# Kernel optimization log

Hardware: AMD Instinct MI355X
Metric: run time of the kernel (lower is better)

## Reference

```python
import jax, jax.numpy as jnp
import numpy as np

C_IN = 1024
C_MID = 512  # in_channels // shrink_factor


def conv1x1(x, w, b):
    # x: [B, Cin, H, W], w: [Cout, Cin], b: [Cout]
    return jnp.einsum('bchw,oc->bohw', x, w) + b[None, :, None, None]


def setup_inputs() -> dict:
    key = jax.random.key(0)
    ks = jax.random.split(key, 9)
    B, H, W = 8, 48, 48
    x = jax.random.normal(ks[0], (B, C_IN, H, W), dtype=jnp.float32)
    s = 0.02
    w1 = jax.random.normal(ks[1], (C_MID, C_IN), dtype=jnp.float32) * s
    b1 = jnp.zeros((C_MID,), dtype=jnp.float32)
    w2 = jax.random.normal(ks[2], (C_MID, C_IN), dtype=jnp.float32) * s
    b2 = jnp.zeros((C_MID,), dtype=jnp.float32)
    w3 = jax.random.normal(ks[3], (C_MID, C_IN), dtype=jnp.float32) * s
    b3 = jnp.zeros((C_MID,), dtype=jnp.float32)
    w4 = jax.random.normal(ks[4], (C_IN, C_MID), dtype=jnp.float32) * s
    b4 = jnp.zeros((C_IN,), dtype=jnp.float32)
    return {'x': x, 'w1': w1, 'b1': b1, 'w2': w2, 'b2': b2,
            'w3': w3, 'b3': b3, 'w4': w4, 'b4': b4}


def reference(x, w1, b1, w2, b2, w3, b3, w4, b4):
    B, C, H, W = x.shape
    # 1x1 conv projections (theta, phi, g), each [B, C_MID, H, W]
    x_theta = conv1x1(x, w1, b1)
    x_phi = conv1x1(x, w2, b2)
    x_g = conv1x1(x, w3, b3)
    # NOTE: the original uses raw .view() (no transpose); torch and jnp are both
    # row-major, so jnp.reshape reproduces the exact same memory reinterpretation.
    x_g = x_g.reshape(B, -1, C_MID)      # [B, N, C_MID]
    x_theta = x_theta.reshape(B, -1, C_MID)  # [B, N, C_MID]
    x_phi = x_phi.reshape(B, C_MID, -1)  # [B, C_MID, N]
    # full dense N x N affinity (N = H*W)
    att = jnp.einsum('bnc,bcm->bnm', x_theta, x_phi)
    att = jax.nn.softmax(att, axis=-1)
    y = jnp.einsum('bnm,bmc->bnc', att, x_g)  # [B, N, C_MID]
    y = y.reshape(B, C_MID, H, W)
    x_last = conv1x1(y, w4, b4)  # [B, C_IN, H, W]
    return x + x_last
```

## Files before the change

### kernel.cpp

```cpp
#include <hip/hip_runtime.h>

typedef unsigned short u16;
typedef __bf16 bf16x8_t __attribute__((ext_vector_type(8)));
typedef float f32x4_t __attribute__((ext_vector_type(4)));

__device__ __forceinline__ u16 f2bf(float f) {
  unsigned u = __builtin_bit_cast(unsigned, f);
  u += 0x7FFFu + ((u >> 16) & 1u);
  return (u16)(u >> 16);
}
__device__ __forceinline__ float bf2f(u16 h) {
  unsigned u = ((unsigned)h) << 16;
  return __builtin_bit_cast(float, u);
}

typedef __attribute__((address_space(1))) const unsigned gas_u32;
typedef __attribute__((address_space(3))) unsigned las_u32;
__device__ __forceinline__ void gload16(const void* g, void* l) {
  __builtin_amdgcn_global_load_lds((gas_u32*)g, (las_u32*)l, 16, 0, 0);
}

#define SBAR()                                  \
  do {                                          \
    __builtin_amdgcn_sched_barrier(0);          \
    asm volatile("" ::: "memory");              \
    __builtin_amdgcn_s_barrier();               \
    asm volatile("" ::: "memory");              \
    __builtin_amdgcn_sched_barrier(0);          \
  } while (0)
#define VM10() asm volatile("s_waitcnt vmcnt(10)" ::: "memory")
#define VM12() asm volatile("s_waitcnt vmcnt(12)" ::: "memory")

__global__ __launch_bounds__(256) void cast4_kernel(
    const float* __restrict__ a0, const float* __restrict__ a1,
    const float* __restrict__ a2, const float* __restrict__ a3,
    u16* __restrict__ out) {
  const int z = blockIdx.z;
  const float* a = (z == 0) ? a0 : (z == 1) ? a1 : (z == 2) ? a2 : a3;
  const int i = blockIdx.x * 256 + threadIdx.x;
  out[(size_t)z * 524288 + i] = f2bf(a[i]);
}

__global__ __launch_bounds__(256) void bcat_kernel(
    const float* __restrict__ b1, const float* __restrict__ b3,
    float* __restrict__ o) {
  const int i = blockIdx.x * 256 + threadIdx.x;
  o[i] = (i < 512) ? b1[i] : b3[i - 512];
}

__global__ __launch_bounds__(256) void cast_transpose_kernel(
    const float* __restrict__ in, u16* __restrict__ out, int R, int C,
    long sIn, long sOut) {
  __shared__ u16 t[32][33];
  const int b = blockIdx.z;
  in += (long)b * sIn;
  out += (long)b * sOut;
  const int c0 = blockIdx.x * 32, r0 = blockIdx.y * 32;
  const int tx = threadIdx.x, ty = threadIdx.y;
#pragma unroll
  for (int i = 0; i < 32; i += 8)
    t[ty + i][tx] = f2bf(in[(long)(r0 + ty + i) * C + c0 + tx]);
  __syncthreads();
#pragma unroll
  for (int i = 0; i < 32; i += 8)
    out[(long)(c0 + ty + i) * R + r0 + tx] = t[tx][ty + i];
}

__global__ __launch_bounds__(256) void transpose64(
    const u16* __restrict__ in, u16* __restrict__ out, int R, int C, long sIn,
    long sOut) {
  __shared__ u16 t[64][66];
  const int b = blockIdx.z;
  in += (long)b * sIn;
  out += (long)b * sOut;
  const int c0 = blockIdx.x * 64, r0 = blockIdx.y * 64;
  const int tx = threadIdx.x & 31, ty = threadIdx.x >> 5;
#pragma unroll
  for (int i = 0; i < 64; i += 8) {
    unsigned v = *(const unsigned*)&in[(long)(r0 + ty + i) * C + c0 + 2 * tx];
    t[ty + i][2 * tx] = (u16)v;
    t[ty + i][2 * tx + 1] = (u16)(v >> 16);
  }
  __syncthreads();
#pragma unroll
  for (int i = 0; i < 64; i += 8) {
    unsigned lo = t[2 * tx][ty + i], hi = t[2 * tx + 1][ty + i];
    *(unsigned*)&out[(long)(c0 + ty + i) * R + r0 + 2 * tx] = lo | (hi << 16);
  }
}

#define STG_A(bufv, h, kt)                                          \
  do {                                                              \
    const char* g_ = Ag + (size_t)(kt) * 128 + (size_t)(h)*AH;      \
    char* d_ = sAd + (bufv)*32768 + (h)*16384;                      \
    gload16(g_, d_);                                                \
    gload16(g_ + AC, d_ + 8192);                                    \
  } while (0)
#define STG_B(bufv, h, kt)                                          \
  do {                                                              \
    const char* g_ = Bg + (size_t)(kt) * 128 + (size_t)(h)*BH;      \
    char* d_ = sBd + (bufv)*32768 + (h)*16384;                      \
    gload16(g_, d_);                                                \
    gload16(g_ + BC, d_ + 8192);                                    \
  } while (0)
#define LOAD_A(bufv, mh)                                                     \
  _Pragma("unroll") for (int m = 0; m < 4; m++) {                            \
    const int lr_ = (mh)*128 + wr * 64 + m * 16 + l15;                       \
    af[m][0] = *(const bf16x8_t*)(lds + (bufv)*32768 + lr_ * 128 + koff0);   \
    af[m][1] =                                                               \
        *(const bf16x8_t*)(lds + (bufv)*32768 + lr_ * 128 + (koff0 ^ 64));   \
  }
#define LOAD_B(bufv, nh)                                                     \
  _Pragma("unroll") for (int n = 0; n < 2; n++) {                            \
    const int lr_ = (nh)*128 + wc * 32 + n * 16 + l15;                       \
    bfr[(nh)*2 + n][0] =                                                     \
        *(const bf16x8_t*)(lds + 65536 + (bufv)*32768 + lr_ * 128 + koff0);  \
    bfr[(nh)*2 + n][1] = *(const bf16x8_t*)(lds + 65536 + (bufv)*32768 +     \
                                            lr_ * 128 + (koff0 ^ 64));       \
  }
#define MMA(mh, nh)                                                          \
  __builtin_amdgcn_s_setprio(1);                                            \
  _Pragma("unroll") for (int m = 0; m < 4; m++)                              \
      _Pragma("unroll") for (int n = 0; n < 2; n++)                          \
          _Pragma("unroll") for (int kk = 0; kk < 2; kk++)                   \
              acc[(mh)*4 + m][(nh)*2 + n] =                                  \
      __builtin_amdgcn_mfma_f32_16x16x32_bf16(                               \
          af[m][kk], bfr[(nh)*2 + n][kk], acc[(mh)*4 + m][(nh)*2 + n], 0, 0, \
          0);                                                                \
  __builtin_amdgcn_s_setprio(0);

template <int MODE>
__global__ __launch_bounds__(512, 2) void gemm8(
    const u16* __restrict__ A, const u16* __restrict__ B,
    void* __restrict__ C0, void* __restrict__ C1, void* __restrict__ C2,
    const u16* __restrict__ W2, const float* __restrict__ bias,
    const float* __restrict__ bias2, const float* __restrict__ resid,
    float* __restrict__ stats) {
  constexpr int LDA_ = (MODE == 0) ? 1024 : (MODE == 3) ? 2304 : 512;
  constexpr int LDB_ = (MODE == 0) ? 1024 : (MODE == 3) ? 2304 : 512;
  constexpr int KK = (MODE == 0) ? 1024 : (MODE == 3) ? 2304 : 512;
  constexpr int NT = KK >> 6;
  constexpr size_t AH = 64ull * LDA_ * 2, AC = 128ull * LDA_ * 2;
  constexpr size_t BH = 32ull * LDB_ * 2, BC = 128ull * LDB_ * 2;

  __shared__ alignas(16) char lds[131072];
  const int tid = threadIdx.x;
  const int w = tid >> 6, l = tid & 63;
  const int wr = w >> 2, wc = w & 3;
  const int l15 = l & 15, lhi = l >> 4;
  const int koff0 = (lhi * 16) ^ ((l & 7) << 4);

  unsigned bx, by, bz;
  bool roleB = false;
  if constexpr (MODE == 0) {
    unsigned bid = blockIdx.x;
    unsigned swz = (bid & 7u) * 54u + (bid >> 3);
    roleB = (swz >= 288u);
    unsigned s = roleB ? swz - 288u : swz;
    if (roleB) { bx = s % 2u; by = (s / 2u) % 9u; bz = s / 18u; }
    else       { bx = s % 9u; by = (s / 9u) % 4u; bz = s / 36u; }
  } else {
    const unsigned gx = gridDim.x, gy = gridDim.y;
    const unsigned nb = gx * gy * gridDim.z;
    unsigned bid = blockIdx.x + gx * (blockIdx.y + gy * blockIdx.z);
    bid = (bid & 7u) * (nb >> 3) + (bid >> 3);
    bx = bid % gx;
    unsigned t1 = bid / gx;
    by = t1 % gy;
    bz = t1 / gy;
  }
  const int rowbase = by * 256, colbase = bx * 256;

  const u16* Abase;
  const u16* Bbase;
  if constexpr (MODE == 0) {
    Abase = roleB ? (B + (size_t)bz * 2359296) : A;
    Bbase = roleB ? W2 : (B + (size_t)bz * 2359296);
  } else if constexpr (MODE == 1) {
    Abase = A + (size_t)bz * 1179648;
    Bbase = B + (size_t)bz * 1179648;
  } else if constexpr (MODE == 3) {
    Abase = A + (size_t)bz * 5308416;
    Bbase = B + (size_t)bz * 1179648;
  } else {
    Abase = A;
    Bbase = B + (size_t)bz * 1179648;
  }

  const int sub = tid >> 3;
  const int kb = ((tid & 7) * 16) ^ ((sub & 7) << 4);
  const char* Ag = (const char*)(Abase + (size_t)(rowbase + sub) * LDA_) + kb;
  const char* Bg =
      (const char*)(Bbase + (size_t)(colbase + (sub >> 5) * 64 + (sub & 31)) *
                                LDB_) +
      kb;
  char* sAd = lds + w * 1024;
  char* sBd = lds + 65536 + w * 1024;

  f32x4_t acc[8][4] = {};
  bf16x8_t af[4][2], bfr[4][2];

  STG_A(0, 0, 0); STG_B(0, 0, 0);
  STG_B(0, 1, 0); STG_A(0, 1, 0);
  STG_A(1, 0, 1); STG_B(1, 0, 1);
  STG_B(1, 1, 1); STG_A(1, 1, 1);
  VM12();
  SBAR();

  for (int t = 0; t < NT; ++t) {
    const int c = t & 1;
    const int tn2 = (t + 2 < NT) ? t + 2 : NT - 1;
    LOAD_A(c, 0);
    LOAD_B(c, 0);
    SBAR();
    MMA(0, 0);
    VM10();
    SBAR();
    LOAD_B(c, 1);
    STG_A(c, 0, tn2);
    STG_B(c, 0, tn2);
    SBAR();
    MMA(0, 1);
    VM12();
    SBAR();
    LOAD_A(c, 1);
    STG_B(c, 1, tn2);
    SBAR();
    MMA(1, 0);
    SBAR();
    STG_A(c, 1, tn2);
    VM12();
    SBAR();
    MMA(1, 1);
    SBAR();
  }

  if constexpr (MODE == 0) {
    if (!roleB) {
      const int rb = rowbase + wr * 128;
      const int which = rb >> 9;
      u16* Cp = (u16*)(which ? C1 : C0) + (size_t)bz * 1179648;
      const int rowout0 = rb - which * 512;
#pragma unroll
      for (int mf = 0; mf < 8; mf++)
#pragma unroll
        for (int r = 0; r < 4; r++) {
          const int ro = mf * 16 + lhi * 4 + r;
          const float bv = bias[rb + ro];
          const size_t rowo = (size_t)(rowout0 + ro) * 2304;
#pragma unroll
          for (int nf = 0; nf < 4; nf++) {
            const int col = colbase + wc * 64 + nf * 16 + l15;
            Cp[rowo + col] = f2bf(acc[mf][nf][r] + bv);
          }
        }
    } else {
      u16* Cp = (u16*)C2 + (size_t)bz * 1179648;
#pragma unroll
      for (int mf = 0; mf < 8; mf++)
#pragma unroll
        for (int r = 0; r < 4; r++) {
          const size_t rowo =
              (size_t)(rowbase + wr * 128 + mf * 16 + lhi * 4 + r) * 512;
#pragma unroll
          for (int nf = 0; nf < 4; nf++) {
            const int col = colbase + wc * 64 + nf * 16 + l15;
            Cp[rowo + col] = f2bf(acc[mf][nf][r] + bias2[col]);
          }
        }
    }
  } else if constexpr (MODE == 1) {
    u16* Cp = (u16*)C0 + (size_t)bz * 5308416;
#pragma unroll
    for (int mf = 0; mf < 8; mf++)
#pragma unroll
      for (int r = 0; r < 4; r++) {
        const int row = rowbase + wr * 128 + mf * 16 + lhi * 4 + r;
        float sm = 0.f;
#pragma unroll
        for (int nf = 0; nf < 4; nf++) {
          const int col = colbase + wc * 64 + nf * 16 + l15;
          const u16 hb = f2bf(__expf(acc[mf][nf][r]));
          Cp[(size_t)row * 2304 + col] = hb;
          sm += bf2f(hb);
        }
#pragma unroll
        for (int mk = 1; mk < 16; mk <<= 1) sm += __shfl_xor(sm, mk);
        if (l15 == 0)
          stats[((size_t)bz * 36 + bx * 4 + wc) * 2304 + row] = sm;
      }
  } else if constexpr (MODE == 3) {
    u16* Cp = (u16*)C0 + (size_t)bz * 1179648;
#pragma unroll
    for (int mf = 0; mf < 8; mf++)
#pragma unroll
      for (int r = 0; r < 4; r++) {
        const int row = rowbase + wr * 128 + mf * 16 + lhi * 4 + r;
        const float invs = stats[(size_t)bz * 2304 + row];
#pragma unroll
        for (int nf = 0; nf < 4; nf++) {
          const int col = colbase + wc * 64 + nf * 16 + l15;
          Cp[(size_t)row * 512 + col] = f2bf(acc[mf][nf][r] * invs);
        }
      }
  } else {
    float* Cp = (float*)C0 + (size_t)bz * 2359296;
    const float* rp = resid + (size_t)bz * 2359296;
#pragma unroll
    for (int mf = 0; mf < 8; mf++)
#pragma unroll
      for (int r = 0; r < 4; r++) {
        const int row = rowbase + wr * 128 + mf * 16 + lhi * 4 + r;
        const float bv = bias[row];
#pragma unroll
        for (int nf = 0; nf < 4; nf++) {
          const int col = colbase + wc * 64 + nf * 16 + l15;
          Cp[(size_t)row * 2304 + col] =
              acc[mf][nf][r] + bv + rp[(size_t)row * 2304 + col];
        }
      }
  }
}

__global__ __launch_bounds__(256) void reduce_sums(
    const float* __restrict__ stats, float* __restrict__ rowinv) {
  const int i = blockIdx.x * 256 + threadIdx.x;
  const int bz = i / 2304, n = i % 2304;
  const float* s = stats + (size_t)bz * 36 * 2304 + n;
  float S = 0.f;
  for (int j = 0; j < 36; j++) S += s[(size_t)j * 2304];
  rowinv[i] = 1.0f / S;
}

extern "C" void kernel_launch(void* const* d_in, const int* in_sizes, int n_in,
                              void* d_out, int out_size, void* d_ws,
                              size_t ws_size, hipStream_t stream) {
  const float* x = (const float*)d_in[0];
  const float* w1 = (const float*)d_in[1];
  const float* b1 = (const float*)d_in[2];
  const float* w2 = (const float*)d_in[3];
  const float* b2 = (const float*)d_in[4];
  const float* w3 = (const float*)d_in[5];
  const float* b3 = (const float*)d_in[6];
  const float* w4 = (const float*)d_in[7];
  const float* b4 = (const float*)d_in[8];
  float* out = (float*)d_out;
  char* ws = (char*)d_ws;

  if (ws_size < 268435456ull) return;
  u16* p_xT = (u16*)(ws);
  u16* p_gn = (u16*)(ws + 37748736);
  float* p_bcat = (float*)(ws + 56623104);
  u16* p_att = (u16*)(ws);
  float* p_stats = (float*)(ws + 84934656);
  float* p_rinv = (float*)(ws + 87588864);
  u16* p_wb = (u16*)(ws + 169869312);
  u16* p_theta = (u16*)(ws + 174063616);
  u16* p_phiT = (u16*)(ws + 192937984);
  u16* p_gT = (u16*)(ws + 211812352);
  u16* p_y = (u16*)(ws + 230686720);
  u16* p_yrT = (u16*)(ws + 249561088);

  cast4_kernel<<<dim3(2048, 1, 4), 256, 0, stream>>>(w1, w3, w2, w4, p_wb);
  bcat_kernel<<<dim3(4), 256, 0, stream>>>(b1, b3, p_bcat);
  cast_transpose_kernel<<<dim3(72, 32, 8), dim3(32, 8), 0, stream>>>(
      x, p_xT, 1024, 2304, 2359296L, 2359296L);
  gemm8<0><<<dim3(432), 512, 0, stream>>>(
      p_wb, p_xT, p_theta, p_gn, p_phiT, p_wb + 1048576, p_bcat, b2, nullptr,
      nullptr);
  transpose64<<<dim3(8, 36, 8), 256, 0, stream>>>(p_gn, p_gT, 2304, 512,
                                                  1179648L, 1179648L);
  gemm8<1><<<dim3(9, 9, 8), 512, 0, stream>>>(
      p_theta, p_phiT, p_att, nullptr, nullptr, nullptr, nullptr, nullptr,
      nullptr, p_stats);
  reduce_sums<<<dim3(72), 256, 0, stream>>>(p_stats, p_rinv);
  gemm8<3><<<dim3(2, 9, 8), 512, 0, stream>>>(
      p_att, p_gT, p_y, nullptr, nullptr, nullptr, nullptr, nullptr, nullptr,
      p_rinv);
  transpose64<<<dim3(36, 8, 8), 256, 0, stream>>>(p_y, p_yrT, 512, 2304,
                                                  1179648L, 1179648L);
  gemm8<2><<<dim3(9, 4, 8), 512, 0, stream>>>(
      p_wb + 1572864, p_yrT, out, nullptr, nullptr, nullptr, b4, nullptr, x,
      nullptr);
}
```

Baseline: 309.9 us.

## Stage GEMM epilogues through LDS for coalesced vector global stores

All GEMM epilogue modes now write accumulator tiles into LDS first, then read them back as 16-byte vectors, so each global store (and the fp32 residual load) is fully coalesced instead of scattered 2- or 4-byte writes. The exp-softmax mode also computes row partial sums over the whole 256-column block tile, cutting the stats partials from 36 to 9 per row, and the reduction kernel is updated to match. This adds LDS round trips, extra barriers and a full vmcnt drain before the epilogue.

```diff
diff --git a/kernel.cpp b/kernel.cpp
--- a/kernel.cpp
+++ b/kernel.cpp
@@ -2,6 +2,7 @@
 
 typedef unsigned short u16;
 typedef __bf16 bf16x8_t __attribute__((ext_vector_type(8)));
+typedef unsigned short u16x8_t __attribute__((ext_vector_type(8)));
 typedef float f32x4_t __attribute__((ext_vector_type(4)));
 
 __device__ __forceinline__ u16 f2bf(float f) {
@@ -28,8 +29,10 @@
     asm volatile("" ::: "memory");              \
     __builtin_amdgcn_sched_barrier(0);          \
   } while (0)
+#define VM0() asm volatile("s_waitcnt vmcnt(0)" ::: "memory")
 #define VM10() asm volatile("s_waitcnt vmcnt(10)" ::: "memory")
 #define VM12() asm volatile("s_waitcnt vmcnt(12)" ::: "memory")
+#define LGKM0() asm volatile("s_waitcnt lgkmcnt(0)" ::: "memory")
 
 __global__ __launch_bounds__(256) void cast4_kernel(
     const float* __restrict__ a0, const float* __restrict__ a1,
@@ -235,90 +238,122 @@
     SBAR();
   }
 
-  if constexpr (MODE == 0) {
-    if (!roleB) {
-      const int rb = rowbase + wr * 128;
-      const int which = rb >> 9;
-      u16* Cp = (u16*)(which ? C1 : C0) + (size_t)bz * 1179648;
-      const int rowout0 = rb - which * 512;
-#pragma unroll
-      for (int mf = 0; mf < 8; mf++)
+  VM0();
+  SBAR();
+
+  if constexpr (MODE == 2) {
+    constexpr int PF = 264;
+    float* ebf = (float*)lds;
+    float* Cp = (float*)C0 + (size_t)bz * 2359296;
+    const float* rp = resid + (size_t)bz * 2359296;
+#pragma unroll
+    for (int h = 0; h < 4; ++h) {
+#pragma unroll
+      for (int m2 = 0; m2 < 2; m2++) {
+        const int mf = h * 2 + m2;
 #pragma unroll
         for (int r = 0; r < 4; r++) {
-          const int ro = mf * 16 + lhi * 4 + r;
-          const float bv = bias[rb + ro];
-          const size_t rowo = (size_t)(rowout0 + ro) * 2304;
+          const int lr = wr * 32 + m2 * 16 + lhi * 4 + r;
+          const float bv = bias[rowbase + wr * 128 + mf * 16 + lhi * 4 + r];
+#pragma unroll
+          for (int nf = 0; nf < 4; nf++)
+            ebf[lr * PF + wc * 64 + nf * 16 + l15] = acc[mf][nf][r] + bv;
+        }
+      }
+      LGKM0();
+      SBAR();
+#pragma unroll
+      for (int i = 0; i < 8; i++) {
+        const int flat = i * 512 + tid;
+        const int rr = flat >> 6, cg = flat & 63;
+        f32x4_t v = *(const f32x4_t*)&ebf[rr * PF + cg * 4];
+        const int ro = (rr >> 5) * 128 + h * 32 + (rr & 31);
+        const size_t gidx = (size_t)(rowbase + ro) * 2304 + colbase + cg * 4;
+        const f32x4_t rv = *(const f32x4_t*)&rp[gidx];
+        v[0] += rv[0]; v[1] += rv[1]; v[2] += rv[2]; v[3] += rv[3];
+        *(f32x4_t*)&Cp[gidx] = v;
+      }
+      SBAR();
+    }
+  } else {
+    constexpr int P = 272;
+    u16* eb = (u16*)lds;
+    u16* Cp;
+    int ldc, rowout0;
+    if constexpr (MODE == 0) {
+      if (!roleB) {
+        const int which = rowbase >> 9;
+        Cp = (u16*)(which ? C1 : C0) + (size_t)bz * 1179648;
+        ldc = 2304;
+        rowout0 = rowbase - which * 512;
+      } else {
+        Cp = (u16*)C2 + (size_t)bz * 1179648;
+        ldc = 512;
+        rowout0 = rowbase;
+      }
+    } else if constexpr (MODE == 1) {
+      Cp = (u16*)C0 + (size_t)bz * 5308416;
+      ldc = 2304;
+      rowout0 = rowbase;
+    } else {
+      Cp = (u16*)C0 + (size_t)bz * 1179648;
+      ldc = 512;
+      rowout0 = rowbase;
+    }
+#pragma unroll
+    for (int h = 0; h < 2; ++h) {
+#pragma unroll
+      for (int m2 = 0; m2 < 4; m2++) {
+        const int mf = h * 4 + m2;
+#pragma unroll
+        for (int r = 0; r < 4; r++) {
+          const int lr = wr * 64 + m2 * 16 + lhi * 4 + r;
+          const int ro = wr * 128 + mf * 16 + lhi * 4 + r;
+          float addv = 0.f, mulv = 1.f;
+          if constexpr (MODE == 0) {
+            if (!roleB) addv = bias[rowbase + ro];
+          } else if constexpr (MODE == 3) {
+            mulv = stats[(size_t)bz * 2304 + rowbase + ro];
+          }
 #pragma unroll
           for (int nf = 0; nf < 4; nf++) {
-            const int col = colbase + wc * 64 + nf * 16 + l15;
-            Cp[rowo + col] = f2bf(acc[mf][nf][r] + bv);
+            const int col = wc * 64 + nf * 16 + l15;
+            float v = acc[mf][nf][r];
+            if constexpr (MODE == 1)
+              v = __expf(v);
+            else if constexpr (MODE == 3)
+              v = v * mulv;
+            else if constexpr (MODE == 0) {
+              if (roleB)
+                v += bias2[colbase + col];
+              else
+                v += addv;
+            }
+            eb[lr * P + col] = f2bf(v);
           }
         }
-    } else {
-      u16* Cp = (u16*)C2 + (size_t)bz * 1179648;
-#pragma unroll
-      for (int mf = 0; mf < 8; mf++)
-#pragma unroll
-        for (int r = 0; r < 4; r++) {
-          const size_t rowo =
-              (size_t)(rowbase + wr * 128 + mf * 16 + lhi * 4 + r) * 512;
-#pragma unroll
-          for (int nf = 0; nf < 4; nf++) {
-            const int col = colbase + wc * 64 + nf * 16 + l15;
-            Cp[rowo + col] = f2bf(acc[mf][nf][r] + bias2[col]);
-          }
-        }
-    }
-  } else if constexpr (MODE == 1) {
-    u16* Cp = (u16*)C0 + (size_t)bz * 5308416;
-#pragma unroll
-    for (int mf = 0; mf < 8; mf++)
-#pragma unroll
-      for (int r = 0; r < 4; r++) {
-        const int row = rowbase + wr * 128 + mf * 16 + lhi * 4 + r;
-        float sm = 0.f;
-#pragma unroll
-        for (int nf = 0; nf < 4; nf++) {
-          const int col = colbase + wc * 64 + nf * 16 + l15;
-          const u16 hb = f2bf(__expf(acc[mf][nf][r]));
-          Cp[(size_t)row * 2304 + col] = hb;
-          sm += bf2f(hb);
-        }
-#pragma unroll
-        for (int mk = 1; mk < 16; mk <<= 1) sm += __shfl_xor(sm, mk);
-        if (l15 == 0)
-          stats[((size_t)bz * 36 + bx * 4 + wc) * 2304 + row] = sm;
       }
-  } else if constexpr (MODE == 3) {
-    u16* Cp = (u16*)C0 + (size_t)bz * 1179648;
-#pragma unroll
-    for (int mf = 0; mf < 8; mf++)
-#pragma unroll
-      for (int r = 0; r < 4; r++) {
-        const int row = rowbase + wr * 128 + mf * 16 + lhi * 4 + r;
-        const float invs = stats[(size_t)bz * 2304 + row];
-#pragma unroll
-        for (int nf = 0; nf < 4; nf++) {
-          const int col = colbase + wc * 64 + nf * 16 + l15;
-          Cp[(size_t)row * 512 + col] = f2bf(acc[mf][nf][r] * invs);
+      LGKM0();
+      SBAR();
+#pragma unroll
+      for (int i = 0; i < 8; i++) {
+        const int flat = i * 512 + tid;
+        const int rr = flat >> 5, cg = flat & 31;
+        u16x8_t v = *(const u16x8_t*)&eb[rr * P + cg * 8];
+        const int ro = (rr >> 6) * 128 + h * 64 + (rr & 63);
+        *(u16x8_t*)&Cp[(size_t)(rowout0 + ro) * ldc + colbase + cg * 8] = v;
+        if constexpr (MODE == 1) {
+          float s8 = 0.f;
+#pragma unroll
+          for (int j = 0; j < 8; j++) s8 += bf2f(v[j]);
+#pragma unroll
+          for (int o = 1; o < 32; o <<= 1) s8 += __shfl_xor(s8, o);
+          if ((l & 31) == 0)
+            stats[((size_t)bz * 9 + bx) * 2304 + rowbase + ro] = s8;
         }
       }
-  } else {
-    float* Cp = (float*)C0 + (size_t)bz * 2359296;
-    const float* rp = resid + (size_t)bz * 2359296;
-#pragma unroll
-    for (int mf = 0; mf < 8; mf++)
-#pragma unroll
-      for (int r = 0; r < 4; r++) {
-        const int row = rowbase + wr * 128 + mf * 16 + lhi * 4 + r;
-        const float bv = bias[row];
-#pragma unroll
-        for (int nf = 0; nf < 4; nf++) {
-          const int col = colbase + wc * 64 + nf * 16 + l15;
-          Cp[(size_t)row * 2304 + col] =
-              acc[mf][nf][r] + bv + rp[(size_t)row * 2304 + col];
-        }
-      }
+      SBAR();
+    }
   }
 }
 
@@ -326,9 +361,9 @@
     const float* __restrict__ stats, float* __restrict__ rowinv) {
   const int i = blockIdx.x * 256 + threadIdx.x;
   const int bz = i / 2304, n = i % 2304;
-  const float* s = stats + (size_t)bz * 36 * 2304 + n;
+  const float* s = stats + (size_t)bz * 9 * 2304 + n;
   float S = 0.f;
-  for (int j = 0; j < 36; j++) S += s[(size_t)j * 2304];
+  for (int j = 0; j < 9; j++) S += s[(size_t)j * 2304];
   rowinv[i] = 1.0f / S;
 }
 
```

Measured after the change: 316.7 us. 2.2% more time.

## Merge prep kernels, fold g-transpose into attention GEMM, fuse row-sum reduction

Applied to the files above, without the earlier changes.

Combines the weight cast, bias concat and x cast-transpose into one launch. The g transpose now runs as extra blocks inside the attention-score GEMM launch, and the softmax row-sum reduction moves into the epilogue of the att·g GEMM through LDS. This removes four kernel launches and the separate reduce pass, at the cost of each MODE 3 block re-reading 36 partial sums per row.

```diff
diff --git a/kernel.cpp b/kernel.cpp
--- a/kernel.cpp
+++ b/kernel.cpp
@@ -28,42 +28,43 @@
     asm volatile("" ::: "memory");              \
     __builtin_amdgcn_sched_barrier(0);          \
   } while (0)
+#define VM0() asm volatile("s_waitcnt vmcnt(0)" ::: "memory")
 #define VM10() asm volatile("s_waitcnt vmcnt(10)" ::: "memory")
 #define VM12() asm volatile("s_waitcnt vmcnt(12)" ::: "memory")
-
-__global__ __launch_bounds__(256) void cast4_kernel(
-    const float* __restrict__ a0, const float* __restrict__ a1,
-    const float* __restrict__ a2, const float* __restrict__ a3,
-    u16* __restrict__ out) {
-  const int z = blockIdx.z;
-  const float* a = (z == 0) ? a0 : (z == 1) ? a1 : (z == 2) ? a2 : a3;
-  const int i = blockIdx.x * 256 + threadIdx.x;
-  out[(size_t)z * 524288 + i] = f2bf(a[i]);
-}
-
-__global__ __launch_bounds__(256) void bcat_kernel(
-    const float* __restrict__ b1, const float* __restrict__ b3,
-    float* __restrict__ o) {
-  const int i = blockIdx.x * 256 + threadIdx.x;
-  o[i] = (i < 512) ? b1[i] : b3[i - 512];
-}
-
-__global__ __launch_bounds__(256) void cast_transpose_kernel(
-    const float* __restrict__ in, u16* __restrict__ out, int R, int C,
-    long sIn, long sOut) {
-  __shared__ u16 t[32][33];
-  const int b = blockIdx.z;
-  in += (long)b * sIn;
-  out += (long)b * sOut;
-  const int c0 = blockIdx.x * 32, r0 = blockIdx.y * 32;
-  const int tx = threadIdx.x, ty = threadIdx.y;
-#pragma unroll
-  for (int i = 0; i < 32; i += 8)
-    t[ty + i][tx] = f2bf(in[(long)(r0 + ty + i) * C + c0 + tx]);
-  __syncthreads();
-#pragma unroll
-  for (int i = 0; i < 32; i += 8)
-    out[(long)(c0 + ty + i) * R + r0 + tx] = t[tx][ty + i];
+#define LGKM0() asm volatile("s_waitcnt lgkmcnt(0)" ::: "memory")
+
+__global__ __launch_bounds__(256) void prep_kernel(
+    const float* __restrict__ x, const float* __restrict__ w1,
+    const float* __restrict__ w3, const float* __restrict__ w2,
+    const float* __restrict__ w4, const float* __restrict__ b1,
+    const float* __restrict__ b3, u16* __restrict__ xT, u16* __restrict__ wb,
+    float* __restrict__ bcat) {
+  const unsigned idx = blockIdx.x;
+  const int tid = threadIdx.x;
+  if (idx < 18432u) {
+    __shared__ u16 t[32][33];
+    const int xx = idx % 72, yy = (idx / 72) % 32, b = idx / 2304;
+    const float* in = x + (size_t)b * 2359296;
+    u16* out = xT + (size_t)b * 2359296;
+    const int c0 = xx * 32, r0 = yy * 32;
+    const int tx = tid & 31, ty = tid >> 5;
+#pragma unroll
+    for (int i = 0; i < 32; i += 8)
+      t[ty + i][tx] = f2bf(in[(size_t)(r0 + ty + i) * 2304 + c0 + tx]);
+    __syncthreads();
+#pragma unroll
+    for (int i = 0; i < 32; i += 8)
+      out[(size_t)(c0 + ty + i) * 1024 + r0 + tx] = t[tx][ty + i];
+  } else if (idx < 26624u) {
+    const unsigned k = idx - 18432u;
+    const int z = k >> 11;
+    const float* a = (z == 0) ? w1 : (z == 1) ? w3 : (z == 2) ? w2 : w4;
+    const int i = (int)(k & 2047u) * 256 + tid;
+    wb[(size_t)z * 524288 + i] = f2bf(a[i]);
+  } else {
+    const int i = (int)(idx - 26624u) * 256 + tid;
+    if (i < 1024) bcat[i] = (i < 512) ? b1[i] : b3[i - 512];
+  }
 }
 
 __global__ __launch_bounds__(256) void transpose64(
@@ -129,13 +130,48 @@
           0);                                                                \
   __builtin_amdgcn_s_setprio(0);
 
+#define MAINLOOP(NTv)                                                        \
+  STG_A(0, 0, 0); STG_B(0, 0, 0);                                            \
+  STG_B(0, 1, 0); STG_A(0, 1, 0);                                            \
+  STG_A(1, 0, 1); STG_B(1, 0, 1);                                            \
+  STG_B(1, 1, 1); STG_A(1, 1, 1);                                            \
+  VM12();                                                                    \
+  SBAR();                                                                    \
+  for (int t = 0; t < (NTv); ++t) {                                          \
+    const int c = t & 1;                                                     \
+    const int tn2 = (t + 2 < (NTv)) ? t + 2 : (NTv)-1;                       \
+    LOAD_A(c, 0);                                                            \
+    LOAD_B(c, 0);                                                            \
+    SBAR();                                                                  \
+    MMA(0, 0);                                                               \
+    VM10();                                                                  \
+    SBAR();                                                                  \
+    LOAD_B(c, 1);                                                            \
+    STG_A(c, 0, tn2);                                                        \
+    STG_B(c, 0, tn2);                                                        \
+    SBAR();                                                                  \
+    MMA(0, 1);                                                               \
+    VM12();                                                                  \
+    SBAR();                                                                  \
+    LOAD_A(c, 1);                                                            \
+    STG_B(c, 1, tn2);                                                        \
+    SBAR();                                                                  \
+    MMA(1, 0);                                                               \
+    SBAR();                                                                  \
+    STG_A(c, 1, tn2);                                                        \
+    VM12();                                                                  \
+    SBAR();                                                                  \
+    MMA(1, 1);                                                               \
+    SBAR();                                                                  \
+  }
+
 template <int MODE>
 __global__ __launch_bounds__(512, 2) void gemm8(
     const u16* __restrict__ A, const u16* __restrict__ B,
     void* __restrict__ C0, void* __restrict__ C1, void* __restrict__ C2,
     const u16* __restrict__ W2, const float* __restrict__ bias,
     const float* __restrict__ bias2, const float* __restrict__ resid,
-    float* __restrict__ stats) {
+    const float* __restrict__ stats) {
   constexpr int LDA_ = (MODE == 0) ? 1024 : (MODE == 3) ? 2304 : 512;
   constexpr int LDB_ = (MODE == 0) ? 1024 : (MODE == 3) ? 2304 : 512;
   constexpr int KK = (MODE == 0) ? 1024 : (MODE == 3) ? 2304 : 512;
@@ -176,9 +212,6 @@
   if constexpr (MODE == 0) {
     Abase = roleB ? (B + (size_t)bz * 2359296) : A;
     Bbase = roleB ? W2 : (B + (size_t)bz * 2359296);
-  } else if constexpr (MODE == 1) {
-    Abase = A + (size_t)bz * 1179648;
-    Bbase = B + (size_t)bz * 1179648;
   } else if constexpr (MODE == 3) {
     Abase = A + (size_t)bz * 5308416;
     Bbase = B + (size_t)bz * 1179648;
@@ -200,40 +233,7 @@
   f32x4_t acc[8][4] = {};
   bf16x8_t af[4][2], bfr[4][2];
 
-  STG_A(0, 0, 0); STG_B(0, 0, 0);
-  STG_B(0, 1, 0); STG_A(0, 1, 0);
-  STG_A(1, 0, 1); STG_B(1, 0, 1);
-  STG_B(1, 1, 1); STG_A(1, 1, 1);
-  VM12();
-  SBAR();
-
-  for (int t = 0; t < NT; ++t) {
-    const int c = t & 1;
-    const int tn2 = (t + 2 < NT) ? t + 2 : NT - 1;
-    LOAD_A(c, 0);
-    LOAD_B(c, 0);
-    SBAR();
-    MMA(0, 0);
-    VM10();
-    SBAR();
-    LOAD_B(c, 1);
-    STG_A(c, 0, tn2);
-    STG_B(c, 0, tn2);
-    SBAR();
-    MMA(0, 1);
-    VM12();
-    SBAR();
-    LOAD_A(c, 1);
-    STG_B(c, 1, tn2);
-    SBAR();
-    MMA(1, 0);
-    SBAR();
-    STG_A(c, 1, tn2);
-    VM12();
-    SBAR();
-    MMA(1, 1);
-    SBAR();
-  }
+  MAINLOOP(NT);
 
   if constexpr (MODE == 0) {
     if (!roleB) {
@@ -269,34 +269,28 @@
           }
         }
     }
-  } else if constexpr (MODE == 1) {
-    u16* Cp = (u16*)C0 + (size_t)bz * 5308416;
+  } else if constexpr (MODE == 3) {
+    VM0();
+    SBAR();
+    float* rsum = (float*)lds;
+    if (tid < 256) {
+      const int row = rowbase + tid;
+      float S = 0.f;
+#pragma unroll 4
+      for (int j = 0; j < 36; j++)
+        S += stats[((size_t)bz * 36 + j) * 2304 + row];
+      rsum[tid] = 1.0f / S;
+    }
+    LGKM0();
+    SBAR();
+    u16* Cp = (u16*)C0 + (size_t)bz * 1179648;
 #pragma unroll
     for (int mf = 0; mf < 8; mf++)
 #pragma unroll
       for (int r = 0; r < 4; r++) {
-        const int row = rowbase + wr * 128 + mf * 16 + lhi * 4 + r;
-        float sm = 0.f;
-#pragma unroll
-        for (int nf = 0; nf < 4; nf++) {
-          const int col = colbase + wc * 64 + nf * 16 + l15;
-          const u16 hb = f2bf(__expf(acc[mf][nf][r]));
-          Cp[(size_t)row * 2304 + col] = hb;
-          sm += bf2f(hb);
-        }
-#pragma unroll
-        for (int mk = 1; mk < 16; mk <<= 1) sm += __shfl_xor(sm, mk);
-        if (l15 == 0)
-          stats[((size_t)bz * 36 + bx * 4 + wc) * 2304 + row] = sm;
-      }
-  } else if constexpr (MODE == 3) {
-    u16* Cp = (u16*)C0 + (size_t)bz * 1179648;
-#pragma unroll
-    for (int mf = 0; mf < 8; mf++)
-#pragma unroll
-      for (int r = 0; r < 4; r++) {
-        const int row = rowbase + wr * 128 + mf * 16 + lhi * 4 + r;
-        const float invs = stats[(size_t)bz * 2304 + row];
+        const int ro = wr * 128 + mf * 16 + lhi * 4 + r;
+        const float invs = rsum[ro];
+        const int row = rowbase + ro;
 #pragma unroll
         for (int nf = 0; nf < 4; nf++) {
           const int col = colbase + wc * 64 + nf * 16 + l15;
@@ -322,14 +316,95 @@
   }
 }
 
-__global__ __launch_bounds__(256) void reduce_sums(
-    const float* __restrict__ stats, float* __restrict__ rowinv) {
-  const int i = blockIdx.x * 256 + threadIdx.x;
-  const int bz = i / 2304, n = i % 2304;
-  const float* s = stats + (size_t)bz * 36 * 2304 + n;
-  float S = 0.f;
-  for (int j = 0; j < 36; j++) S += s[(size_t)j * 2304];
-  rowinv[i] = 1.0f / S;
+__global__ __launch_bounds__(512, 2) void att_fused(
+    const u16* __restrict__ A, const u16* __restrict__ B, u16* __restrict__ C0,
+    float* __restrict__ stats, const u16* __restrict__ gn,
+    u16* __restrict__ gTo) {
+  constexpr int LDA_ = 512, LDB_ = 512, NT = 8;
+  constexpr size_t AH = 64ull * 512 * 2, AC = 128ull * 512 * 2;
+  constexpr size_t BH = 32ull * 512 * 2, BC = 128ull * 512 * 2;
+  __shared__ alignas(16) char lds[131072];
+  const int tid = threadIdx.x;
+
+  if (blockIdx.x >= 648u) {
+    const int t2 = (int)(blockIdx.x - 648u) * 2 + (tid >> 8);
+    const int st = tid & 255;
+    const int tx = st & 31, ty = st >> 5;
+    const int xx = t2 & 7;
+    const int rest = t2 >> 3;
+    const int yy = rest % 36, b = rest / 36;
+    const u16* in = gn + (size_t)b * 1179648;
+    u16* out = gTo + (size_t)b * 1179648;
+    const int c0 = xx * 64, r0 = yy * 64;
+    u16* tt = (u16*)lds + (size_t)(tid >> 8) * 64 * 66;
+#pragma unroll
+    for (int i = 0; i < 64; i += 8) {
+      unsigned v =
+          *(const unsigned*)&in[(size_t)(r0 + ty + i) * 512 + c0 + 2 * tx];
+      tt[(ty + i) * 66 + 2 * tx] = (u16)v;
+      tt[(ty + i) * 66 + 2 * tx + 1] = (u16)(v >> 16);
+    }
+    __syncthreads();
+#pragma unroll
+    for (int i = 0; i < 64; i += 8) {
+      unsigned lo = tt[(2 * tx) * 66 + ty + i];
+      unsigned hi = tt[(2 * tx + 1) * 66 + ty + i];
+      *(unsigned*)&out[(size_t)(c0 + ty + i) * 2304 + r0 + 2 * tx] =
+          lo | (hi << 16);
+    }
+    return;
+  }
+
+  const int w = tid >> 6, l = tid & 63;
+  const int wr = w >> 2, wc = w & 3;
+  const int l15 = l & 15, lhi = l >> 4;
+  const int koff0 = (lhi * 16) ^ ((l & 7) << 4);
+
+  unsigned bid = blockIdx.x;
+  bid = (bid & 7u) * 81u + (bid >> 3);
+  const unsigned bx = bid % 9u;
+  const unsigned t1 = bid / 9u;
+  const unsigned by = t1 % 9u;
+  const unsigned bz = t1 / 9u;
+  const int rowbase = by * 256, colbase = bx * 256;
+
+  const u16* Abase = A + (size_t)bz * 1179648;
+  const u16* Bbase = B + (size_t)bz * 1179648;
+
+  const int sub = tid >> 3;
+  const int kb = ((tid & 7) * 16) ^ ((sub & 7) << 4);
+  const char* Ag = (const char*)(Abase + (size_t)(rowbase + sub) * LDA_) + kb;
+  const char* Bg =
+      (const char*)(Bbase + (size_t)(colbase + (sub >> 5) * 64 + (sub & 31)) *
+                                LDB_) +
+      kb;
+  char* sAd = lds + w * 1024;
+  char* sBd = lds + 65536 + w * 1024;
+
+  f32x4_t acc[8][4] = {};
+  bf16x8_t af[4][2], bfr[4][2];
+
+  MAINLOOP(NT);
+
+  u16* Cp = C0 + (size_t)bz * 5308416;
+#pragma unroll
+  for (int mf = 0; mf < 8; mf++)
+#pragma unroll
+    for (int r = 0; r < 4; r++) {
+      const int row = rowbase + wr * 128 + mf * 16 + lhi * 4 + r;
+      float sm = 0.f;
+#pragma unroll
+      for (int nf = 0; nf < 4; nf++) {
+        const int col = colbase + wc * 64 + nf * 16 + l15;
+        const u16 hb = f2bf(__expf(acc[mf][nf][r]));
+        Cp[(size_t)row * 2304 + col] = hb;
+        sm += bf2f(hb);
+      }
+#pragma unroll
+      for (int mk = 1; mk < 16; mk <<= 1) sm += __shfl_xor(sm, mk);
+      if (l15 == 0)
+        stats[((size_t)bz * 36 + bx * 4 + wc) * 2304 + row] = sm;
+    }
 }
 
 extern "C" void kernel_launch(void* const* d_in, const int* in_sizes, int n_in,
@@ -349,11 +424,10 @@
 
   if (ws_size < 268435456ull) return;
   u16* p_xT = (u16*)(ws);
-  u16* p_gn = (u16*)(ws + 37748736);
   float* p_bcat = (float*)(ws + 56623104);
   u16* p_att = (u16*)(ws);
   float* p_stats = (float*)(ws + 84934656);
-  float* p_rinv = (float*)(ws + 87588864);
+  u16* p_gn = (u16*)(ws + 104857600);
   u16* p_wb = (u16*)(ws + 169869312);
   u16* p_theta = (u16*)(ws + 174063616);
   u16* p_phiT = (u16*)(ws + 192937984);
@@ -361,22 +435,16 @@
   u16* p_y = (u16*)(ws + 230686720);
   u16* p_yrT = (u16*)(ws + 249561088);
 
-  cast4_kernel<<<dim3(2048, 1, 4), 256, 0, stream>>>(w1, w3, w2, w4, p_wb);
-  bcat_kernel<<<dim3(4), 256, 0, stream>>>(b1, b3, p_bcat);
-  cast_transpose_kernel<<<dim3(72, 32, 8), dim3(32, 8), 0, stream>>>(
-      x, p_xT, 1024, 2304, 2359296L, 2359296L);
+  prep_kernel<<<dim3(26628), 256, 0, stream>>>(x, w1, w3, w2, w4, b1, b3,
+                                               p_xT, p_wb, p_bcat);
   gemm8<0><<<dim3(432), 512, 0, stream>>>(
       p_wb, p_xT, p_theta, p_gn, p_phiT, p_wb + 1048576, p_bcat, b2, nullptr,
       nullptr);
-  transpose64<<<dim3(8, 36, 8), 256, 0, stream>>>(p_gn, p_gT, 2304, 512,
-                                                  1179648L, 1179648L);
-  gemm8<1><<<dim3(9, 9, 8), 512, 0, stream>>>(
-      p_theta, p_phiT, p_att, nullptr, nullptr, nullptr, nullptr, nullptr,
-      nullptr, p_stats);
-  reduce_sums<<<dim3(72), 256, 0, stream>>>(p_stats, p_rinv);
+  att_fused<<<dim3(1800), 512, 0, stream>>>(p_theta, p_phiT, p_att, p_stats,
+                                            p_gn, p_gT);
   gemm8<3><<<dim3(2, 9, 8), 512, 0, stream>>>(
       p_att, p_gT, p_y, nullptr, nullptr, nullptr, nullptr, nullptr, nullptr,
-      p_rinv);
+      p_stats);
   transpose64<<<dim3(36, 8, 8), 256, 0, stream>>>(p_y, p_yrT, 512, 2304,
                                                   1179648L, 1179648L);
   gemm8<2><<<dim3(9, 4, 8), 512, 0, stream>>>(
```

Result: faster. 299.4 us (-3.4%).
